# Kernel tuning notes

Hardware: AMD Instinct MI355X
Metric: run time of the kernel (lower is better)

## Reference

```python
import jax, jax.numpy as jnp
import numpy as np

ZERO_THRESH = 1e-20
N_ECC, N_POLAR = 15, 20          # 300 log-polar pooling windows
MIN_ECC, MAX_ECC = 0.5, 15.0      # degrees
NUM_SCALES, N_ORI = 4, 4          # order=3 -> 4 orientations
BASE_RES = 512


def _make_windows(res):
    """Mostly-zero log-polar Gaussian pooling windows, (N_ECC*N_POLAR, res, res)."""
    ys, xs = np.meshgrid(np.arange(res) - res / 2 + 0.5,
                         np.arange(res) - res / 2 + 0.5, indexing='ij')
    deg_per_pix = MAX_ECC / (res / 2)
    r = np.sqrt(xs ** 2 + ys ** 2) * deg_per_pix
    logr = np.log(np.maximum(r, 1e-6))
    theta = np.arctan2(ys, xs)
    mus_e = np.linspace(np.log(MIN_ECC), np.log(MAX_ECC), N_ECC)
    se = mus_e[1] - mus_e[0]
    mus_a = np.linspace(-np.pi, np.pi, N_POLAR, endpoint=False)
    sa = 2 * np.pi / N_POLAR
    dth = ((theta[None] - mus_a[:, None, None] + np.pi) % (2 * np.pi)) - np.pi
    ang = np.exp(-0.5 * (dth / sa) ** 2)                              # (P,H,W)
    rad = np.exp(-0.5 * ((logr[None] - mus_e[:, None, None]) / se) ** 2)  # (E,H,W)
    w = (rad[:, None] * ang[None]).reshape(N_ECC * N_POLAR, res, res)
    w[w < 1e-6] = 0.0   # enforce the sparse (mostly-zero) structure
    return w.astype(np.float32)


def setup_inputs() -> dict:
    key = jax.random.key(0)
    ks = jax.random.split(key, 6)
    inp = {'image': jax.random.uniform(ks[0], (BASE_RES, BASE_RES), dtype=jnp.float32)}
    for s in range(NUM_SCALES):
        res = BASE_RES >> s
        # complex pyramid coefficients: (orientations, H_s, W_s, [real, imag])
        inp[f'pyr{s}'] = jax.random.normal(ks[1 + s], (N_ORI, res, res, 2), dtype=jnp.float32)
        inp[f'win{s}'] = jnp.asarray(_make_windows(res))
    return inp


def reference(image, pyr0, pyr1, pyr2, pyr3, win0, win1, win2, win3):
    img = image[None, None]                       # (1,1,H,W) as in forward's unsqueeze
    parts = []
    for p, w in zip((pyr0, pyr1, pyr2, pyr3), (win0, win1, win2, win3)):
        # complex modulus: sqrt(re^2 + im^2), (O, H_s, W_s)
        m = jnp.sqrt(jnp.sum(p * p, axis=-1))
        # number of non-zero pixels per window
        wnp = jnp.sum(w > ZERO_THRESH, axis=(-1, -2)).astype(m.dtype)   # (W,)
        # windowed sum fused (einsum ijkl,wkl->ijwkl then sum(-1,-2) == direct contraction)
        pooled = jnp.einsum('okl,wkl->ow', m, w) / wnp
        parts.append(pooled.reshape(-1))          # orientation-major, matches dict order
    wnp0 = jnp.sum(win0 > ZERO_THRESH, axis=(-1, -2)).astype(img.dtype)
    mean_lum = (jnp.einsum('ijkl,wkl->ijw', img, win0) / wnp0).reshape(-1)
    return jnp.concatenate(parts + [mean_lum])
```

## Files before the change

kernel.cpp:

```cpp
#include <hip/hip_runtime.h>


#define THREADS 256
#define PPT 8
#define CHUNK (THREADS * PPT)
#define WPG 100
#define N_WIN 300
#define ZTHRESH 1e-20f

#define WS_FLOATS 6300

template <bool HAS_IMG>
__device__ __forceinline__ void pool_scale(const float* __restrict__ pyr,
                                           const float* __restrict__ win,
                                           const float* __restrict__ img,
                                           float* __restrict__ ws,
                                           int HW, int scale, int chunk, int wgrp)
{
    __shared__ float lacc[4][WPG * 6];
    const int tid  = threadIdx.x;
    const int lane = tid & 63;
    const int wave = tid >> 6;

    const size_t pix0 = (size_t)chunk * CHUNK + (size_t)tid * PPT;

    float m[PPT][4];
#pragma unroll
    for (int o = 0; o < 4; ++o) {
        const float4* pp = (const float4*)(pyr + ((size_t)o * HW + pix0) * 2);
#pragma unroll
        for (int j = 0; j < PPT / 2; ++j) {
            float4 v = pp[j];
            m[2 * j][o]     = sqrtf(fmaf(v.x, v.x, v.y * v.y));
            m[2 * j + 1][o] = sqrtf(fmaf(v.z, v.z, v.w * v.w));
        }
    }
    float iv[PPT];
    if (HAS_IMG) {
        const float4* ip = (const float4*)(img + pix0);
#pragma unroll
        for (int j = 0; j < PPT / 4; ++j) {
            float4 v = ip[j];
            iv[4 * j] = v.x; iv[4 * j + 1] = v.y; iv[4 * j + 2] = v.z; iv[4 * j + 3] = v.w;
        }
    }

    const int w0 = wgrp * WPG;

    for (int wi = 0; wi < WPG; ++wi) {
        const int w = w0 + wi;
        const float4* wp = (const float4*)(win + (size_t)w * HW + pix0);
        float wv[PPT];
#pragma unroll
        for (int j = 0; j < PPT / 4; ++j) {
            float4 v = wp[j];
            wv[4 * j] = v.x; wv[4 * j + 1] = v.y; wv[4 * j + 2] = v.z; wv[4 * j + 3] = v.w;
        }
        float a0 = 0.f, a1 = 0.f, a2 = 0.f, a3 = 0.f, ct = 0.f, ia = 0.f;
#pragma unroll
        for (int p = 0; p < PPT; ++p) {
            a0 = fmaf(wv[p], m[p][0], a0);
            a1 = fmaf(wv[p], m[p][1], a1);
            a2 = fmaf(wv[p], m[p][2], a2);
            a3 = fmaf(wv[p], m[p][3], a3);
            ct += (wv[p] > ZTHRESH) ? 1.f : 0.f;
            if (HAS_IMG) ia = fmaf(wv[p], iv[p], ia);
        }
#pragma unroll
        for (int s = 1; s < 64; s <<= 1) {
            a0 += __shfl_xor(a0, s, 64);
            a1 += __shfl_xor(a1, s, 64);
            a2 += __shfl_xor(a2, s, 64);
            a3 += __shfl_xor(a3, s, 64);
            ct += __shfl_xor(ct, s, 64);
            if (HAS_IMG) ia += __shfl_xor(ia, s, 64);
        }
        if (lane == 0) {
            float* slot = &lacc[wave][wi * 6];
            slot[0] = a0; slot[1] = a1; slot[2] = a2; slot[3] = a3;
            slot[4] = ct; slot[5] = HAS_IMG ? ia : 0.f;
        }
    }
    __syncthreads();

    float* sums = ws + (size_t)scale * 1200;
    float* cnt  = ws + 4800 + (size_t)scale * 300;
    float* imgs = ws + 6000;
    for (int i = tid; i < WPG * 6; i += THREADS) {
        float v = lacc[0][i] + lacc[1][i] + lacc[2][i] + lacc[3][i];
        int wi = i / 6, f = i - wi * 6;
        int w = w0 + wi;
        if (f < 4) {
            atomicAdd(&sums[f * 300 + w], v);
        } else if (f == 4) {
            atomicAdd(&cnt[w], v);
        } else if (HAS_IMG) {
            atomicAdd(&imgs[w], v);
        }
    }
}

__global__ __launch_bounds__(THREADS)
void pool_kernel(const float* __restrict__ image,
                 const float* __restrict__ pyr0, const float* __restrict__ win0,
                 const float* __restrict__ pyr1, const float* __restrict__ win1,
                 const float* __restrict__ pyr2, const float* __restrict__ win2,
                 const float* __restrict__ pyr3, const float* __restrict__ win3,
                 float* __restrict__ ws)
{
    int bid = blockIdx.x;
    if (bid < 384) {
        int chunk = bid & 127, wgrp = bid >> 7;
        pool_scale<true>(pyr0, win0, image, ws, 512 * 512, 0, chunk, wgrp);
    } else if (bid < 480) {
        int l = bid - 384;
        int chunk = l & 31, wgrp = l >> 5;
        pool_scale<false>(pyr1, win1, nullptr, ws, 256 * 256, 1, chunk, wgrp);
    } else if (bid < 504) {
        int l = bid - 480;
        int chunk = l & 7, wgrp = l >> 3;
        pool_scale<false>(pyr2, win2, nullptr, ws, 128 * 128, 2, chunk, wgrp);
    } else {
        int l = bid - 504;
        int chunk = l & 1, wgrp = l >> 1;
        pool_scale<false>(pyr3, win3, nullptr, ws, 64 * 64, 3, chunk, wgrp);
    }
}

__global__ __launch_bounds__(THREADS)
void finalize_kernel(const float* __restrict__ ws, float* __restrict__ out)
{
    int i = blockIdx.x * blockDim.x + threadIdx.x;
    if (i >= 5100) return;
    float v;
    if (i < 4800) {
        int s = i / 1200;
        int w = i % 300;
        v = ws[i] / ws[4800 + s * 300 + w];
    } else {
        int w = i - 4800;
        v = ws[6000 + w] / ws[4800 + w];
    }
    out[i] = v;
}

extern "C" void kernel_launch(void* const* d_in, const int* in_sizes, int n_in,
                              void* d_out, int out_size, void* d_ws, size_t ws_size,
                              hipStream_t stream)
{
    const float* image = (const float*)d_in[0];
    const float* pyr0  = (const float*)d_in[1];
    const float* win0  = (const float*)d_in[2];
    const float* pyr1  = (const float*)d_in[3];
    const float* win1  = (const float*)d_in[4];
    const float* pyr2  = (const float*)d_in[5];
    const float* win2  = (const float*)d_in[6];
    const float* pyr3  = (const float*)d_in[7];
    const float* win3  = (const float*)d_in[8];
    float* ws  = (float*)d_ws;
    float* out = (float*)d_out;

    hipMemsetAsync(d_ws, 0, WS_FLOATS * sizeof(float), stream);
    pool_kernel<<<510, THREADS, 0, stream>>>(image, pyr0, win0, pyr1, win1,
                                             pyr2, win2, pyr3, win3, ws);
    finalize_kernel<<<(5100 + THREADS - 1) / THREADS, THREADS, 0, stream>>>(ws, out);
}
```

Before: 537.2 us.

## Halve pixels per thread, double grid, prefetch windows with nontemporal loads

Cuts pixels per thread from 8 to 4 and doubles the grid to 1020 blocks so more waves are in flight while the window tensors are streamed. Window rows are software-prefetched two iterations ahead with nontemporal vector loads to hide memory latency and avoid polluting cache. The nonzero count now comes from a wave ballot plus popcount instead of a float shuffle reduction, which removes one shuffle chain per window. More blocks also means twice as many shared-memory reductions and atomics into the workspace.

New measurement: 566.1 us. 1.05x slower.

```diff
diff --git a/kernel.cpp b/kernel.cpp
--- a/kernel.cpp
+++ b/kernel.cpp
@@ -2,13 +2,14 @@
 
 
 #define THREADS 256
-#define PPT 8
+#define PPT 4
 #define CHUNK (THREADS * PPT)
 #define WPG 100
-#define N_WIN 300
 #define ZTHRESH 1e-20f
 
 #define WS_FLOATS 6300
+
+typedef float fvec4 __attribute__((ext_vector_type(4)));
 
 template <bool HAS_IMG>
 __device__ __forceinline__ void pool_scale(const float* __restrict__ pyr,
@@ -24,62 +25,59 @@
 
     const size_t pix0 = (size_t)chunk * CHUNK + (size_t)tid * PPT;
 
-    float m[PPT][4];
+    float mm[4][PPT];
 #pragma unroll
     for (int o = 0; o < 4; ++o) {
         const float4* pp = (const float4*)(pyr + ((size_t)o * HW + pix0) * 2);
-#pragma unroll
-        for (int j = 0; j < PPT / 2; ++j) {
-            float4 v = pp[j];
-            m[2 * j][o]     = sqrtf(fmaf(v.x, v.x, v.y * v.y));
-            m[2 * j + 1][o] = sqrtf(fmaf(v.z, v.z, v.w * v.w));
-        }
+        float4 v0 = pp[0];
+        float4 v1 = pp[1];
+        mm[o][0] = sqrtf(fmaf(v0.x, v0.x, v0.y * v0.y));
+        mm[o][1] = sqrtf(fmaf(v0.z, v0.z, v0.w * v0.w));
+        mm[o][2] = sqrtf(fmaf(v1.x, v1.x, v1.y * v1.y));
+        mm[o][3] = sqrtf(fmaf(v1.z, v1.z, v1.w * v1.w));
     }
-    float iv[PPT];
-    if (HAS_IMG) {
-        const float4* ip = (const float4*)(img + pix0);
-#pragma unroll
-        for (int j = 0; j < PPT / 4; ++j) {
-            float4 v = ip[j];
-            iv[4 * j] = v.x; iv[4 * j + 1] = v.y; iv[4 * j + 2] = v.z; iv[4 * j + 3] = v.w;
-        }
-    }
+    float4 iv = make_float4(0.f, 0.f, 0.f, 0.f);
+    if (HAS_IMG) iv = *(const float4*)(img + pix0);
 
     const int w0 = wgrp * WPG;
+    const float* wbase = win + pix0;
 
+    fvec4 c0 = __builtin_nontemporal_load((const fvec4*)(wbase + (size_t)(w0 + 0) * HW));
+    fvec4 c1 = __builtin_nontemporal_load((const fvec4*)(wbase + (size_t)(w0 + 1) * HW));
     for (int wi = 0; wi < WPG; ++wi) {
-        const int w = w0 + wi;
-        const float4* wp = (const float4*)(win + (size_t)w * HW + pix0);
-        float wv[PPT];
-#pragma unroll
-        for (int j = 0; j < PPT / 4; ++j) {
-            float4 v = wp[j];
-            wv[4 * j] = v.x; wv[4 * j + 1] = v.y; wv[4 * j + 2] = v.z; wv[4 * j + 3] = v.w;
-        }
-        float a0 = 0.f, a1 = 0.f, a2 = 0.f, a3 = 0.f, ct = 0.f, ia = 0.f;
-#pragma unroll
-        for (int p = 0; p < PPT; ++p) {
-            a0 = fmaf(wv[p], m[p][0], a0);
-            a1 = fmaf(wv[p], m[p][1], a1);
-            a2 = fmaf(wv[p], m[p][2], a2);
-            a3 = fmaf(wv[p], m[p][3], a3);
-            ct += (wv[p] > ZTHRESH) ? 1.f : 0.f;
-            if (HAS_IMG) ia = fmaf(wv[p], iv[p], ia);
-        }
+        fvec4 cn;
+        if (wi + 2 < WPG)
+            cn = __builtin_nontemporal_load((const fvec4*)(wbase + (size_t)(w0 + wi + 2) * HW));
+        else
+            cn = (fvec4)(0.f);
+
+        int ct = __popcll(__ballot(c0.x > ZTHRESH))
+               + __popcll(__ballot(c0.y > ZTHRESH))
+               + __popcll(__ballot(c0.z > ZTHRESH))
+               + __popcll(__ballot(c0.w > ZTHRESH));
+
+        float a0, a1, a2, a3, ia = 0.f;
+        a0 = fmaf(c0.w, mm[0][3], fmaf(c0.z, mm[0][2], fmaf(c0.y, mm[0][1], c0.x * mm[0][0])));
+        a1 = fmaf(c0.w, mm[1][3], fmaf(c0.z, mm[1][2], fmaf(c0.y, mm[1][1], c0.x * mm[1][0])));
+        a2 = fmaf(c0.w, mm[2][3], fmaf(c0.z, mm[2][2], fmaf(c0.y, mm[2][1], c0.x * mm[2][0])));
+        a3 = fmaf(c0.w, mm[3][3], fmaf(c0.z, mm[3][2], fmaf(c0.y, mm[3][1], c0.x * mm[3][0])));
+        if (HAS_IMG)
+            ia = fmaf(c0.w, iv.w, fmaf(c0.z, iv.z, fmaf(c0.y, iv.y, c0.x * iv.x)));
+
 #pragma unroll
         for (int s = 1; s < 64; s <<= 1) {
             a0 += __shfl_xor(a0, s, 64);
             a1 += __shfl_xor(a1, s, 64);
             a2 += __shfl_xor(a2, s, 64);
             a3 += __shfl_xor(a3, s, 64);
-            ct += __shfl_xor(ct, s, 64);
             if (HAS_IMG) ia += __shfl_xor(ia, s, 64);
         }
         if (lane == 0) {
             float* slot = &lacc[wave][wi * 6];
             slot[0] = a0; slot[1] = a1; slot[2] = a2; slot[3] = a3;
-            slot[4] = ct; slot[5] = HAS_IMG ? ia : 0.f;
+            slot[4] = (float)ct; slot[5] = HAS_IMG ? ia : 0.f;
         }
+        c0 = c1; c1 = cn;
     }
     __syncthreads();
 
@@ -109,20 +107,20 @@
                  float* __restrict__ ws)
 {
     int bid = blockIdx.x;
-    if (bid < 384) {
-        int chunk = bid & 127, wgrp = bid >> 7;
+    if (bid < 768) {
+        int chunk = bid & 255, wgrp = bid >> 8;
         pool_scale<true>(pyr0, win0, image, ws, 512 * 512, 0, chunk, wgrp);
-    } else if (bid < 480) {
-        int l = bid - 384;
-        int chunk = l & 31, wgrp = l >> 5;
+    } else if (bid < 960) {
+        int l = bid - 768;
+        int chunk = l & 63, wgrp = l >> 6;
         pool_scale<false>(pyr1, win1, nullptr, ws, 256 * 256, 1, chunk, wgrp);
-    } else if (bid < 504) {
-        int l = bid - 480;
-        int chunk = l & 7, wgrp = l >> 3;
+    } else if (bid < 1008) {
+        int l = bid - 960;
+        int chunk = l & 15, wgrp = l >> 4;
         pool_scale<false>(pyr2, win2, nullptr, ws, 128 * 128, 2, chunk, wgrp);
     } else {
-        int l = bid - 504;
-        int chunk = l & 1, wgrp = l >> 1;
+        int l = bid - 1008;
+        int chunk = l & 3, wgrp = l >> 2;
         pool_scale<false>(pyr3, win3, nullptr, ws, 64 * 64, 3, chunk, wgrp);
     }
 }
@@ -161,7 +159,7 @@
     float* out = (float*)d_out;
 
     hipMemsetAsync(d_ws, 0, WS_FLOATS * sizeof(float), stream);
-    pool_kernel<<<510, THREADS, 0, stream>>>(image, pyr0, win0, pyr1, win1,
-                                             pyr2, win2, pyr3, win3, ws);
+    pool_kernel<<<1020, THREADS, 0, stream>>>(image, pyr0, win0, pyr1, win1,
+                                              pyr2, win2, pyr3, win3, ws);
     finalize_kernel<<<(5100 + THREADS - 1) / THREADS, THREADS, 0, stream>>>(ws, out);
 }
```

## Prefetch window rows two ahead and use transposed butterfly wave reduction

Applied to the files above, without the earlier changes.

Each thread now handles two float4 pixel groups half a chunk apart, so window loads coalesce across lanes. Window loads use nontemporal hints and are software-pipelined two windows ahead, so memory latency is hidden in a kernel that has few blocks. The per-window 6-value wave reduction is replaced by a transpose-style butterfly: the first shuffle stages split the accumulators between lanes, so far fewer shuffles are needed. This keeps more registers live and relies on the shuffle-lane bookkeeping being correct.

Measured after the change: 505.5 us. 1.06x faster.

```diff
diff --git a/kernel.cpp b/kernel.cpp
--- a/kernel.cpp
+++ b/kernel.cpp
@@ -4,11 +4,13 @@
 #define THREADS 256
 #define PPT 8
 #define CHUNK (THREADS * PPT)
+#define HALFPX 1024
 #define WPG 100
-#define N_WIN 300
 #define ZTHRESH 1e-20f
 
 #define WS_FLOATS 6300
+
+typedef float fvec4 __attribute__((ext_vector_type(4)));
 
 template <bool HAS_IMG>
 __device__ __forceinline__ void pool_scale(const float* __restrict__ pyr,
@@ -22,64 +24,86 @@
     const int lane = tid & 63;
     const int wave = tid >> 6;
 
-    const size_t pix0 = (size_t)chunk * CHUNK + (size_t)tid * PPT;
+    const size_t p0 = (size_t)chunk * CHUNK + (size_t)tid * 4;
+    const size_t p1 = p0 + HALFPX;
 
-    float m[PPT][4];
+    float m0[4][4], m1[4][4];
 #pragma unroll
     for (int o = 0; o < 4; ++o) {
-        const float4* pp = (const float4*)(pyr + ((size_t)o * HW + pix0) * 2);
-#pragma unroll
-        for (int j = 0; j < PPT / 2; ++j) {
-            float4 v = pp[j];
-            m[2 * j][o]     = sqrtf(fmaf(v.x, v.x, v.y * v.y));
-            m[2 * j + 1][o] = sqrtf(fmaf(v.z, v.z, v.w * v.w));
-        }
+        const float4* pa = (const float4*)(pyr + ((size_t)o * HW + p0) * 2);
+        float4 v0 = pa[0], v1 = pa[1];
+        m0[o][0] = sqrtf(fmaf(v0.x, v0.x, v0.y * v0.y));
+        m0[o][1] = sqrtf(fmaf(v0.z, v0.z, v0.w * v0.w));
+        m0[o][2] = sqrtf(fmaf(v1.x, v1.x, v1.y * v1.y));
+        m0[o][3] = sqrtf(fmaf(v1.z, v1.z, v1.w * v1.w));
+        const float4* pb = (const float4*)(pyr + ((size_t)o * HW + p1) * 2);
+        float4 w0v = pb[0], w1v = pb[1];
+        m1[o][0] = sqrtf(fmaf(w0v.x, w0v.x, w0v.y * w0v.y));
+        m1[o][1] = sqrtf(fmaf(w0v.z, w0v.z, w0v.w * w0v.w));
+        m1[o][2] = sqrtf(fmaf(w1v.x, w1v.x, w1v.y * w1v.y));
+        m1[o][3] = sqrtf(fmaf(w1v.z, w1v.z, w1v.w * w1v.w));
     }
-    float iv[PPT];
+    fvec4 i0 = (fvec4)(0.f), i1 = (fvec4)(0.f);
     if (HAS_IMG) {
-        const float4* ip = (const float4*)(img + pix0);
-#pragma unroll
-        for (int j = 0; j < PPT / 4; ++j) {
-            float4 v = ip[j];
-            iv[4 * j] = v.x; iv[4 * j + 1] = v.y; iv[4 * j + 2] = v.z; iv[4 * j + 3] = v.w;
-        }
+        i0 = *(const fvec4*)(img + p0);
+        i1 = *(const fvec4*)(img + p1);
     }
 
     const int w0 = wgrp * WPG;
 
+    fvec4 x0 = __builtin_nontemporal_load((const fvec4*)(win + (size_t)(w0 + 0) * HW + p0));
+    fvec4 y0 = __builtin_nontemporal_load((const fvec4*)(win + (size_t)(w0 + 0) * HW + p1));
+    fvec4 x1 = __builtin_nontemporal_load((const fvec4*)(win + (size_t)(w0 + 1) * HW + p0));
+    fvec4 y1 = __builtin_nontemporal_load((const fvec4*)(win + (size_t)(w0 + 1) * HW + p1));
+
+    const bool pb0 = (lane & 1) != 0;
+    const bool pb1 = (lane & 2) != 0;
+    const bool pb2 = (lane & 4) != 0;
+
     for (int wi = 0; wi < WPG; ++wi) {
-        const int w = w0 + wi;
-        const float4* wp = (const float4*)(win + (size_t)w * HW + pix0);
-        float wv[PPT];
-#pragma unroll
-        for (int j = 0; j < PPT / 4; ++j) {
-            float4 v = wp[j];
-            wv[4 * j] = v.x; wv[4 * j + 1] = v.y; wv[4 * j + 2] = v.z; wv[4 * j + 3] = v.w;
+        fvec4 xn = (fvec4)(0.f), yn = (fvec4)(0.f);
+        if (wi + 2 < WPG) {
+            const float* r = win + (size_t)(w0 + wi + 2) * HW;
+            xn = __builtin_nontemporal_load((const fvec4*)(r + p0));
+            yn = __builtin_nontemporal_load((const fvec4*)(r + p1));
         }
+
         float a0 = 0.f, a1 = 0.f, a2 = 0.f, a3 = 0.f, ct = 0.f, ia = 0.f;
 #pragma unroll
-        for (int p = 0; p < PPT; ++p) {
-            a0 = fmaf(wv[p], m[p][0], a0);
-            a1 = fmaf(wv[p], m[p][1], a1);
-            a2 = fmaf(wv[p], m[p][2], a2);
-            a3 = fmaf(wv[p], m[p][3], a3);
-            ct += (wv[p] > ZTHRESH) ? 1.f : 0.f;
-            if (HAS_IMG) ia = fmaf(wv[p], iv[p], ia);
+        for (int j = 0; j < 4; ++j) {
+            float wx = x0[j], wy = y0[j];
+            a0 = fmaf(wy, m1[0][j], fmaf(wx, m0[0][j], a0));
+            a1 = fmaf(wy, m1[1][j], fmaf(wx, m0[1][j], a1));
+            a2 = fmaf(wy, m1[2][j], fmaf(wx, m0[2][j], a2));
+            a3 = fmaf(wy, m1[3][j], fmaf(wx, m0[3][j], a3));
+            ct += (wx > ZTHRESH) ? 1.f : 0.f;
+            ct += (wy > ZTHRESH) ? 1.f : 0.f;
+            if (HAS_IMG) ia = fmaf(wy, i1[j], fmaf(wx, i0[j], ia));
         }
-#pragma unroll
-        for (int s = 1; s < 64; s <<= 1) {
-            a0 += __shfl_xor(a0, s, 64);
-            a1 += __shfl_xor(a1, s, 64);
-            a2 += __shfl_xor(a2, s, 64);
-            a3 += __shfl_xor(a3, s, 64);
-            ct += __shfl_xor(ct, s, 64);
-            if (HAS_IMG) ia += __shfl_xor(ia, s, 64);
-        }
-        if (lane == 0) {
-            float* slot = &lacc[wave][wi * 6];
-            slot[0] = a0; slot[1] = a1; slot[2] = a2; slot[3] = a3;
-            slot[4] = ct; slot[5] = HAS_IMG ? ia : 0.f;
-        }
+
+        float t0 = __shfl_xor(a0, 1, 64);
+        float t1 = __shfl_xor(a1, 1, 64);
+        float t2 = __shfl_xor(a2, 1, 64);
+        float t3 = __shfl_xor(a3, 1, 64);
+        float t4 = __shfl_xor(ct, 1, 64);
+        float t5 = __shfl_xor(ia, 1, 64);
+        float b0 = pb0 ? (a1 + t1) : (a0 + t0);
+        float b1 = pb0 ? (a3 + t3) : (a2 + t2);
+        float b2 = pb0 ? (ia + t5) : (ct + t4);
+        float u0 = __shfl_xor(b0, 2, 64);
+        float u1 = __shfl_xor(b1, 2, 64);
+        float u2 = __shfl_xor(b2, 2, 64);
+        float c0 = pb1 ? (b1 + u1) : (b0 + u0);
+        float c1 = b2 + u2;
+        float v0 = __shfl_xor(c0, 4, 64);
+        float v1 = __shfl_xor(c1, 4, 64);
+        float d  = pb2 ? (c1 + v1) : (c0 + v0);
+        d += __shfl_xor(d, 8, 64);
+        d += __shfl_xor(d, 16, 64);
+        d += __shfl_xor(d, 32, 64);
+        if (lane < 6) lacc[wave][wi * 6 + lane] = d;
+
+        x0 = x1; y0 = y1; x1 = xn; y1 = yn;
     }
     __syncthreads();
 
```
